# Optimization experiments

Hardware: AMD Instinct MI355X
Metric: run time of the kernel (lower is better)

## Reference

```python
import math
import jax, jax.numpy as jnp
import numpy as np

N_STEPS = 4

def rotate_half(x):
    h = x.shape[-1] // 2
    return jnp.concatenate([-x[..., h:], x[..., :h]], axis=-1)

def setup_inputs() -> dict:
    key = jax.random.key(0)
    k0, k1, k2, k3 = jax.random.split(key, 4)
    B, N, F, D = 2, 4096, 512, 64
    features = jax.random.normal(k0, (B, N, F), jnp.float32)
    # standard RoPE tables, shape [N, D]
    inv_freq = 1.0 / (10000.0 ** (jnp.arange(0, D, 2, dtype=jnp.float32) / D))
    ang = jnp.arange(N, dtype=jnp.float32)[:, None] * inv_freq[None, :]  # [N, D/2]
    ang = jnp.concatenate([ang, ang], axis=-1)  # [N, D]
    cos, sin = jnp.cos(ang), jnp.sin(ang)
    # causal mask broadcast to [B, N, N]
    mask = jnp.broadcast_to(jnp.tril(jnp.ones((N, N), bool)), (B, N, N))
    s = 1.0 / math.sqrt(F)
    Wq = jax.random.normal(k1, (F, D), jnp.float32) * s
    Wk = jax.random.normal(k2, (F, D), jnp.float32) * s
    charge_w = jax.random.normal(k3, (F, 1), jnp.float32) * s
    charge_b = jnp.zeros((1,), jnp.float32)
    step_size = jnp.full((1,), 0.5, jnp.float32)
    charge_decay = jnp.full((1,), 0.3, jnp.float32)
    return dict(features=features, cos=cos, sin=sin, mask=mask, Wq=Wq, Wk=Wk,
                charge_w=charge_w, charge_b=charge_b,
                step_size=step_size, charge_decay=charge_decay)

def reference(features, cos, sin, mask, Wq, Wk, charge_w, charge_b, step_size, charge_decay):
    d_k = Wq.shape[-1]
    Q = jnp.einsum('bnf,fd->bnd', features, Wq)
    K = jnp.einsum('bnf,fd->bnd', features, Wk)
    c, s = cos[None, :, :], sin[None, :, :]  # broadcast over batch
    Q = Q * c + rotate_half(Q) * s
    K = K * c + rotate_half(K) * s
    compat = jnp.einsum('bnd,bmd->bnm', Q, K) / math.sqrt(d_k)  # [B,N,N]
    charge = jax.nn.sigmoid(jnp.einsum('bnf,fo->bno', features, charge_w)[..., 0] + charge_b[0])  # [B,N]
    neg_inf = jnp.asarray(-jnp.inf, compat.dtype)
    logits = jnp.where(mask, compat, neg_inf)
    ss = step_size[0]
    cd = charge_decay[0]
    for _ in range(N_STEPS):
        attn = jax.nn.softmax(logits, axis=-1)
        received = attn.sum(axis=-2)  # column sums, [B,N]
        charge = charge * (1.0 - cd * jax.nn.sigmoid(received - 1.0))
        energy = -compat * charge[..., :, None] * charge[..., None, :]
        logits = jnp.where(mask, logits - ss * energy, neg_inf)
    return jax.nn.softmax(logits, axis=-1)
```

## Files before the change

### kernel.cpp

```cpp
#include <hip/hip_runtime.h>
#include <math.h>

#define NTOK   4096
#define NFEAT  512
#define NDIM   64
#define RROWS  8
#define NBANDS (NTOK / RROWS)

__device__ __forceinline__ float block_max256(float v, float* s) {
#pragma unroll
  for (int o = 32; o > 0; o >>= 1) v = fmaxf(v, __shfl_down(v, o, 64));
  int tid = threadIdx.x;
  if ((tid & 63) == 0) s[tid >> 6] = v;
  __syncthreads();
  v = fmaxf(fmaxf(s[0], s[1]), fmaxf(s[2], s[3]));
  __syncthreads();
  return v;
}
__device__ __forceinline__ float block_sum256(float v, float* s) {
#pragma unroll
  for (int o = 32; o > 0; o >>= 1) v += __shfl_down(v, o, 64);
  int tid = threadIdx.x;
  if ((tid & 63) == 0) s[tid >> 6] = v;
  __syncthreads();
  v = s[0] + s[1] + s[2] + s[3];
  __syncthreads();
  return v;
}

__global__ __launch_bounds__(256) void qk_kernel(
    const float* __restrict__ feat, const float* __restrict__ cosb,
    const float* __restrict__ sinb, const float* __restrict__ Wq,
    const float* __restrict__ Wk, const float* __restrict__ cw,
    const float* __restrict__ cbp, float* __restrict__ Q, float* __restrict__ K,
    float* __restrict__ cur, float* __restrict__ chist)
{
  __shared__ __align__(16) float smem[32 * NFEAT];
  const int tid  = threadIdx.x;
  const int row0 = blockIdx.x * 32;

  const float* fb = feat + (size_t)row0 * NFEAT;
  for (int i = tid; i < 32 * NFEAT; i += 256) {
    int r = i >> 9, c = i & 511;
    smem[(r << 9) + (c ^ ((r & 7) << 2))] = fb[i];
  }
  if (tid < 128) chist[row0 * 4 + tid] = 0.f;
  __syncthreads();

  const int r  = tid >> 3;
  const int cg = tid & 7;
  const int sw = (r & 7) << 2;
  const float* fr = smem + (r << 9);

  float accq[8] = {0, 0, 0, 0, 0, 0, 0, 0};
  float acck[8] = {0, 0, 0, 0, 0, 0, 0, 0};
  float accc = 0.f;
  for (int k = 0; k < NFEAT; ++k) {
    float fv = fr[k ^ sw];
    const float4 wq0 = *(const float4*)(Wq + k * NDIM + cg * 8);
    const float4 wq1 = *(const float4*)(Wq + k * NDIM + cg * 8 + 4);
    const float4 wk0 = *(const float4*)(Wk + k * NDIM + cg * 8);
    const float4 wk1 = *(const float4*)(Wk + k * NDIM + cg * 8 + 4);
    accq[0] = fmaf(fv, wq0.x, accq[0]); accq[1] = fmaf(fv, wq0.y, accq[1]);
    accq[2] = fmaf(fv, wq0.z, accq[2]); accq[3] = fmaf(fv, wq0.w, accq[3]);
    accq[4] = fmaf(fv, wq1.x, accq[4]); accq[5] = fmaf(fv, wq1.y, accq[5]);
    accq[6] = fmaf(fv, wq1.z, accq[6]); accq[7] = fmaf(fv, wq1.w, accq[7]);
    acck[0] = fmaf(fv, wk0.x, acck[0]); acck[1] = fmaf(fv, wk0.y, acck[1]);
    acck[2] = fmaf(fv, wk0.z, acck[2]); acck[3] = fmaf(fv, wk0.w, acck[3]);
    acck[4] = fmaf(fv, wk1.x, acck[4]); acck[5] = fmaf(fv, wk1.y, acck[5]);
    acck[6] = fmaf(fv, wk1.z, acck[6]); acck[7] = fmaf(fv, wk1.w, acck[7]);
    accc = fmaf(fv, cw[k], accc);
  }
  __syncthreads();

  float* sraw = smem;
#pragma unroll
  for (int j = 0; j < 8; ++j) {
    sraw[r * 132 + cg * 8 + j]      = accq[j];
    sraw[r * 132 + 64 + cg * 8 + j] = acck[j];
  }
  if (cg == 0) {
    float cb = cbp[0];
    cur[row0 + r] = 1.f / (1.f + __expf(-(accc + cb)));
  }
  __syncthreads();

  for (int i = tid; i < 32 * NDIM; i += 256) {
    int rr = i >> 6, d = i & 63;
    int g = row0 + rr, n = g & (NTOK - 1);
    float cv = cosb[(n << 6) + d], sv = sinb[(n << 6) + d];
    float qv = sraw[rr * 132 + d];
    float qr = (d < 32) ? -sraw[rr * 132 + d + 32] : sraw[rr * 132 + d - 32];
    Q[(size_t)g * NDIM + d] = qv * cv + qr * sv;
    float kv = sraw[rr * 132 + 64 + d];
    float kr = (d < 32) ? -sraw[rr * 132 + 64 + d + 32] : sraw[rr * 132 + 64 + d - 32];
    K[(size_t)g * NDIM + d] = kv * cv + kr * sv;
  }
}

__global__ __launch_bounds__(256) void compat_kernel(
    const float* __restrict__ Q, const float* __restrict__ K, float* __restrict__ C)
{
  __shared__ __align__(16) float Qs[32][132];
  __shared__ __align__(16) float Ks[32][132];
  int p = blockIdx.x, b = 0;
  if (p >= 528) { b = 1; p -= 528; }
  int ti = (int)((sqrtf(8.f * p + 1.f) - 1.f) * 0.5f);
  while ((ti + 1) * (ti + 2) / 2 <= p) ++ti;
  while (ti * (ti + 1) / 2 > p) --ti;
  int tj = p - ti * (ti + 1) / 2;

  const int tid = threadIdx.x;
  const int ty = tid >> 4, tx = tid & 15;
  const int i0 = ty * 8, j0 = tx * 8;
  const size_t qbase = ((size_t)b * NTOK + (size_t)ti * 128) * NDIM;
  const size_t kbase = ((size_t)b * NTOK + (size_t)tj * 128) * NDIM;

  float acc[8][8];
#pragma unroll
  for (int ii = 0; ii < 8; ++ii)
#pragma unroll
    for (int jj = 0; jj < 8; ++jj) acc[ii][jj] = 0.f;

  for (int dk = 0; dk < NDIM; dk += 32) {
    __syncthreads();
    for (int i = tid; i < 128 * 32; i += 256) {
      int row = i >> 5, d = i & 31;
      Qs[d][row] = Q[qbase + (size_t)row * NDIM + dk + d];
      Ks[d][row] = K[kbase + (size_t)row * NDIM + dk + d];
    }
    __syncthreads();
#pragma unroll
    for (int d = 0; d < 32; ++d) {
      float4 a0 = *(const float4*)&Qs[d][i0];
      float4 a1 = *(const float4*)&Qs[d][i0 + 4];
      float4 b0 = *(const float4*)&Ks[d][j0];
      float4 b1 = *(const float4*)&Ks[d][j0 + 4];
      float av[8] = {a0.x, a0.y, a0.z, a0.w, a1.x, a1.y, a1.z, a1.w};
      float bv[8] = {b0.x, b0.y, b0.z, b0.w, b1.x, b1.y, b1.z, b1.w};
#pragma unroll
      for (int ii = 0; ii < 8; ++ii)
#pragma unroll
        for (int jj = 0; jj < 8; ++jj)
          acc[ii][jj] = fmaf(av[ii], bv[jj], acc[ii][jj]);
    }
  }
#pragma unroll
  for (int ii = 0; ii < 8; ++ii) {
    size_t grow = (size_t)b * NTOK + (size_t)ti * 128 + i0 + ii;
    float4 w0 = make_float4(acc[ii][0] * 0.125f, acc[ii][1] * 0.125f,
                            acc[ii][2] * 0.125f, acc[ii][3] * 0.125f);
    float4 w1 = make_float4(acc[ii][4] * 0.125f, acc[ii][5] * 0.125f,
                            acc[ii][6] * 0.125f, acc[ii][7] * 0.125f);
    *(float4*)&C[grow * NTOK + (size_t)tj * 128 + j0]     = w0;
    *(float4*)&C[grow * NTOK + (size_t)tj * 128 + j0 + 4] = w1;
  }
}

template <int MODE>
__global__ __launch_bounds__(256) void pass_kernel(
    const float* __restrict__ compat, const float4* __restrict__ chist,
    const float* __restrict__ ssp, float* __restrict__ partial,
    float* __restrict__ out)
{
  __shared__ float sred[4];
  const int tid = threadIdx.x;
  int band = blockIdx.x, b = 0;
  if (band >= NBANDS) { b = 1; band -= NBANDS; }
  const int n0 = band * RROWS;
  const float ss = ssp[0];

  float4 ch[16];
#pragma unroll
  for (int k = 0; k < 16; ++k) ch[k] = chist[(b << 12) + tid + (k << 8)];

  float cs[16];
#pragma unroll
  for (int k = 0; k < 16; ++k) cs[k] = 0.f;

  for (int rr = 0; rr < RROWS; ++rr) {
    const int n = n0 + rr;
    const float* rowp = compat + ((size_t)((b << 12) + n) << 12);
    float4 h = chist[(b << 12) + n];
    h.x *= ss; h.y *= ss; h.z *= ss; h.w *= ss;

    float e[16];
    float vmax = -INFINITY;
#pragma unroll
    for (int k = 0; k < 16; ++k) {
      const int col = tid + (k << 8);
      float x = -INFINITY;
      if (col <= n) {
        float cv  = rowp[col];
        float dot = fmaf(ch[k].x, h.x,
                    fmaf(ch[k].y, h.y, fmaf(ch[k].z, h.z, ch[k].w * h.w)));
        x = fmaf(cv, dot, cv);
      }
      e[k] = x;
      vmax = fmaxf(vmax, x);
    }
    float M = block_max256(vmax, sred);
    float lsum = 0.f;
#pragma unroll
    for (int k = 0; k < 16; ++k) {
      float v = __expf(e[k] - M);
      e[k] = v;
      lsum += v;
    }
    float L = block_sum256(lsum, sred);
    float inv = 1.f / L;
    if (MODE == 0) {
#pragma unroll
      for (int k = 0; k < 16; ++k) cs[k] += e[k] * inv;
    } else {
      float* orow = out + ((size_t)((b << 12) + n) << 12);
#pragma unroll
      for (int k = 0; k < 16; ++k) orow[tid + (k << 8)] = e[k] * inv;
    }
  }
  if (MODE == 0) {
    float* pp = partial + ((size_t)b * NBANDS + band) * NTOK;
    const int cmax = n0 + RROWS - 1;
    const int kb = cmax >> 8;
    for (int k = 0; k <= kb; ++k) {
      int col = tid + (k << 8);
      if (col <= cmax) pp[col] = cs[k];
    }
  }
}

__global__ __launch_bounds__(256) void reduce_update_kernel(
    const float* __restrict__ partial, const float* __restrict__ cdp,
    float* __restrict__ cur, float* __restrict__ chist, int step)
{
  __shared__ float s[4][64];
  const int tid = threadIdx.x;
  const int b = blockIdx.x >> 6;
  const int m0 = (blockIdx.x & 63) << 6;
  const int ml = tid & 63, seg = tid >> 6;
  const int m = m0 + ml;
  const int bmin = m >> 3;
  float sum = 0.f;
  const float* pb = partial + (size_t)b * NBANDS * NTOK + m;
  for (int band = bmin + seg; band < NBANDS; band += 4)
    sum += pb[(size_t)band << 12];
  s[seg][ml] = sum;
  __syncthreads();
  if (seg == 0) {
    float r = s[0][ml] + s[1][ml] + s[2][ml] + s[3][ml];
    float sg = 1.f / (1.f + __expf(-(r - 1.f)));
    float cd = cdp[0];
    int idx = (b << 12) + m;
    float c = cur[idx] * (1.f - cd * sg);
    cur[idx] = c;
    chist[idx * 4 + step] = c;
  }
}

extern "C" void kernel_launch(void* const* d_in, const int* in_sizes, int n_in,
                              void* d_out, int out_size, void* d_ws, size_t ws_size,
                              hipStream_t stream) {
  const float* feat = (const float*)d_in[0];
  const float* cosb = (const float*)d_in[1];
  const float* sinb = (const float*)d_in[2];
  const float* Wq  = (const float*)d_in[4];
  const float* Wk  = (const float*)d_in[5];
  const float* cw  = (const float*)d_in[6];
  const float* cbp = (const float*)d_in[7];
  const float* ssp = (const float*)d_in[8];
  const float* cdp = (const float*)d_in[9];
  float* out = (float*)d_out;

  float* ws      = (float*)d_ws;
  float* Q       = ws;
  float* K       = ws + 524288;
  float* chist   = ws + 1048576;
  float* cur     = ws + 1081344;
  float* partial = ws + 1089536;

  qk_kernel<<<256, 256, 0, stream>>>(feat, cosb, sinb, Wq, Wk, cw, cbp, Q, K, cur, chist);
  compat_kernel<<<1056, 256, 0, stream>>>(Q, K, out);
  for (int t = 0; t < 4; ++t) {
    pass_kernel<0><<<2 * NBANDS, 256, 0, stream>>>(out, (const float4*)chist, ssp, partial, nullptr);
    reduce_update_kernel<<<128, 256, 0, stream>>>(partial, cdp, cur, chist, t);
  }
  pass_kernel<1><<<2 * NBANDS, 256, 0, stream>>>(out, (const float4*)chist, ssp, nullptr, out);
}
```

Baseline: 813.3 us.

## Skip masked column chunks in softmax passes and repartition QK and reduce kernels

The softmax pass kernels now compute a per-band upper chunk index and skip loads, exps and stores for 256-column chunks lying entirely above the causal diagonal. The final pass writes zeros for those chunks directly. The QK projection kernel uses 8-row blocks with each thread computing four Q or K outputs, giving four times as many blocks. The column-sum reduction is split across twice as many blocks. The aim is to cut wasted work on masked entries and to raise parallelism in the smaller kernels, at the cost of more runtime branching inside the unrolled loops.

```diff
diff --git a/kernel.cpp b/kernel.cpp
--- a/kernel.cpp
+++ b/kernel.cpp
@@ -35,57 +35,52 @@
     const float* __restrict__ cbp, float* __restrict__ Q, float* __restrict__ K,
     float* __restrict__ cur, float* __restrict__ chist)
 {
-  __shared__ __align__(16) float smem[32 * NFEAT];
+  __shared__ __align__(16) float smem[RROWS * NFEAT];
   const int tid  = threadIdx.x;
-  const int row0 = blockIdx.x * 32;
-
-  const float* fb = feat + (size_t)row0 * NFEAT;
-  for (int i = tid; i < 32 * NFEAT; i += 256) {
-    int r = i >> 9, c = i & 511;
-    smem[(r << 9) + (c ^ ((r & 7) << 2))] = fb[i];
-  }
-  if (tid < 128) chist[row0 * 4 + tid] = 0.f;
-  __syncthreads();
-
-  const int r  = tid >> 3;
-  const int cg = tid & 7;
-  const int sw = (r & 7) << 2;
+  const int row0 = blockIdx.x * RROWS;
+
+  const float4* fb4 = (const float4*)(feat + (size_t)row0 * NFEAT);
+  float4* sm4 = (float4*)smem;
+#pragma unroll
+  for (int i = tid; i < RROWS * NFEAT / 4; i += 256) sm4[i] = fb4[i];
+  if (tid < RROWS * 4) chist[row0 * 4 + tid] = 0.f;
+  __syncthreads();
+
+  const int r   = tid >> 5;
+  const int c   = tid & 31;
+  const int isQ = (c < 16);
+  const int d0  = (c & 15) * 4;
+  const float* __restrict__ Wp = isQ ? Wq : Wk;
   const float* fr = smem + (r << 9);
 
-  float accq[8] = {0, 0, 0, 0, 0, 0, 0, 0};
-  float acck[8] = {0, 0, 0, 0, 0, 0, 0, 0};
+  float a0 = 0.f, a1 = 0.f, a2 = 0.f, a3 = 0.f;
+  for (int k = 0; k < NFEAT; ++k) {
+    float fv = fr[k];
+    float4 w = *(const float4*)(Wp + k * NDIM + d0);
+    a0 = fmaf(fv, w.x, a0); a1 = fmaf(fv, w.y, a1);
+    a2 = fmaf(fv, w.z, a2); a3 = fmaf(fv, w.w, a3);
+  }
+
   float accc = 0.f;
-  for (int k = 0; k < NFEAT; ++k) {
-    float fv = fr[k ^ sw];
-    const float4 wq0 = *(const float4*)(Wq + k * NDIM + cg * 8);
-    const float4 wq1 = *(const float4*)(Wq + k * NDIM + cg * 8 + 4);
-    const float4 wk0 = *(const float4*)(Wk + k * NDIM + cg * 8);
-    const float4 wk1 = *(const float4*)(Wk + k * NDIM + cg * 8 + 4);
-    accq[0] = fmaf(fv, wq0.x, accq[0]); accq[1] = fmaf(fv, wq0.y, accq[1]);
-    accq[2] = fmaf(fv, wq0.z, accq[2]); accq[3] = fmaf(fv, wq0.w, accq[3]);
-    accq[4] = fmaf(fv, wq1.x, accq[4]); accq[5] = fmaf(fv, wq1.y, accq[5]);
-    accq[6] = fmaf(fv, wq1.z, accq[6]); accq[7] = fmaf(fv, wq1.w, accq[7]);
-    acck[0] = fmaf(fv, wk0.x, acck[0]); acck[1] = fmaf(fv, wk0.y, acck[1]);
-    acck[2] = fmaf(fv, wk0.z, acck[2]); acck[3] = fmaf(fv, wk0.w, acck[3]);
-    acck[4] = fmaf(fv, wk1.x, acck[4]); acck[5] = fmaf(fv, wk1.y, acck[5]);
-    acck[6] = fmaf(fv, wk1.z, acck[6]); acck[7] = fmaf(fv, wk1.w, acck[7]);
-    accc = fmaf(fv, cw[k], accc);
-  }
-  __syncthreads();
-
-  float* sraw = smem;
-#pragma unroll
-  for (int j = 0; j < 8; ++j) {
-    sraw[r * 132 + cg * 8 + j]      = accq[j];
-    sraw[r * 132 + 64 + cg * 8 + j] = acck[j];
-  }
-  if (cg == 0) {
+#pragma unroll
+  for (int j = 0; j < 16; ++j) accc = fmaf(fr[c + (j << 5)], cw[c + (j << 5)], accc);
+#pragma unroll
+  for (int o = 16; o > 0; o >>= 1) accc += __shfl_down(accc, o, 64);
+  if (c == 0) {
     float cb = cbp[0];
     cur[row0 + r] = 1.f / (1.f + __expf(-(accc + cb)));
   }
   __syncthreads();
 
-  for (int i = tid; i < 32 * NDIM; i += 256) {
+  float* sraw = smem;
+  {
+    float* dst = sraw + r * 132 + (isQ ? 0 : 64) + d0;
+    dst[0] = a0; dst[1] = a1; dst[2] = a2; dst[3] = a3;
+  }
+  __syncthreads();
+
+#pragma unroll
+  for (int i = tid; i < RROWS * NDIM; i += 256) {
     int rr = i >> 6, d = i & 63;
     int g = row0 + rr, n = g & (NTOK - 1);
     float cv = cosb[(n << 6) + d], sv = sinb[(n << 6) + d];
@@ -132,12 +127,12 @@
     __syncthreads();
 #pragma unroll
     for (int d = 0; d < 32; ++d) {
-      float4 a0 = *(const float4*)&Qs[d][i0];
-      float4 a1 = *(const float4*)&Qs[d][i0 + 4];
-      float4 b0 = *(const float4*)&Ks[d][j0];
-      float4 b1 = *(const float4*)&Ks[d][j0 + 4];
-      float av[8] = {a0.x, a0.y, a0.z, a0.w, a1.x, a1.y, a1.z, a1.w};
-      float bv[8] = {b0.x, b0.y, b0.z, b0.w, b1.x, b1.y, b1.z, b1.w};
+      float4 q0 = *(const float4*)&Qs[d][i0];
+      float4 q1 = *(const float4*)&Qs[d][i0 + 4];
+      float4 k0 = *(const float4*)&Ks[d][j0];
+      float4 k1 = *(const float4*)&Ks[d][j0 + 4];
+      float av[8] = {q0.x, q0.y, q0.z, q0.w, q1.x, q1.y, q1.z, q1.w};
+      float bv[8] = {k0.x, k0.y, k0.z, k0.w, k1.x, k1.y, k1.z, k1.w};
 #pragma unroll
       for (int ii = 0; ii < 8; ++ii)
 #pragma unroll
@@ -168,11 +163,13 @@
   int band = blockIdx.x, b = 0;
   if (band >= NBANDS) { b = 1; band -= NBANDS; }
   const int n0 = band * RROWS;
+  const int kmax = (n0 + RROWS - 1) >> 8;
   const float ss = ssp[0];
 
   float4 ch[16];
 #pragma unroll
-  for (int k = 0; k < 16; ++k) ch[k] = chist[(b << 12) + tid + (k << 8)];
+  for (int k = 0; k < 16; ++k)
+    if (k <= kmax) ch[k] = chist[(b << 12) + tid + (k << 8)];
 
   float cs[16];
 #pragma unroll
@@ -188,6 +185,7 @@
     float vmax = -INFINITY;
 #pragma unroll
     for (int k = 0; k < 16; ++k) {
+      if (k > kmax) continue;
       const int col = tid + (k << 8);
       float x = -INFINITY;
       if (col <= n) {
@@ -203,6 +201,7 @@
     float lsum = 0.f;
 #pragma unroll
     for (int k = 0; k < 16; ++k) {
+      if (k > kmax) continue;
       float v = __expf(e[k] - M);
       e[k] = v;
       lsum += v;
@@ -211,18 +210,23 @@
     float inv = 1.f / L;
     if (MODE == 0) {
 #pragma unroll
-      for (int k = 0; k < 16; ++k) cs[k] += e[k] * inv;
+      for (int k = 0; k < 16; ++k)
+        if (k <= kmax) cs[k] += e[k] * inv;
     } else {
       float* orow = out + ((size_t)((b << 12) + n) << 12);
 #pragma unroll
-      for (int k = 0; k < 16; ++k) orow[tid + (k << 8)] = e[k] * inv;
+      for (int k = 0; k < 16; ++k) {
+        if (k <= kmax) orow[tid + (k << 8)] = e[k] * inv;
+        else           orow[tid + (k << 8)] = 0.f;
+      }
     }
   }
   if (MODE == 0) {
     float* pp = partial + ((size_t)b * NBANDS + band) * NTOK;
     const int cmax = n0 + RROWS - 1;
-    const int kb = cmax >> 8;
-    for (int k = 0; k <= kb; ++k) {
+#pragma unroll
+    for (int k = 0; k < 16; ++k) {
+      if (k > kmax) continue;
       int col = tid + (k << 8);
       if (col <= cmax) pp[col] = cs[k];
     }
@@ -233,21 +237,22 @@
     const float* __restrict__ partial, const float* __restrict__ cdp,
     float* __restrict__ cur, float* __restrict__ chist, int step)
 {
-  __shared__ float s[4][64];
+  __shared__ float s[8][32];
   const int tid = threadIdx.x;
-  const int b = blockIdx.x >> 6;
-  const int m0 = (blockIdx.x & 63) << 6;
-  const int ml = tid & 63, seg = tid >> 6;
+  const int b = blockIdx.x >> 7;
+  const int m0 = (blockIdx.x & 127) << 5;
+  const int ml = tid & 31, seg = tid >> 5;
   const int m = m0 + ml;
   const int bmin = m >> 3;
   float sum = 0.f;
   const float* pb = partial + (size_t)b * NBANDS * NTOK + m;
-  for (int band = bmin + seg; band < NBANDS; band += 4)
+  for (int band = bmin + seg; band < NBANDS; band += 8)
     sum += pb[(size_t)band << 12];
   s[seg][ml] = sum;
   __syncthreads();
   if (seg == 0) {
-    float r = s[0][ml] + s[1][ml] + s[2][ml] + s[3][ml];
+    float r = s[0][ml] + s[1][ml] + s[2][ml] + s[3][ml] +
+              s[4][ml] + s[5][ml] + s[6][ml] + s[7][ml];
     float sg = 1.f / (1.f + __expf(-(r - 1.f)));
     float cd = cdp[0];
     int idx = (b << 12) + m;
@@ -278,11 +283,11 @@
   float* cur     = ws + 1081344;
   float* partial = ws + 1089536;
 
-  qk_kernel<<<256, 256, 0, stream>>>(feat, cosb, sinb, Wq, Wk, cw, cbp, Q, K, cur, chist);
+  qk_kernel<<<1024, 256, 0, stream>>>(feat, cosb, sinb, Wq, Wk, cw, cbp, Q, K, cur, chist);
   compat_kernel<<<1056, 256, 0, stream>>>(Q, K, out);
   for (int t = 0; t < 4; ++t) {
     pass_kernel<0><<<2 * NBANDS, 256, 0, stream>>>(out, (const float4*)chist, ssp, partial, nullptr);
-    reduce_update_kernel<<<128, 256, 0, stream>>>(partial, cdp, cur, chist, t);
+    reduce_update_kernel<<<256, 256, 0, stream>>>(partial, cdp, cur, chist, t);
   }
   pass_kernel<1><<<2 * NBANDS, 256, 0, stream>>>(out, (const float4*)chist, ssp, nullptr, out);
 }
```

After: 732.8 us. 1.11x faster.
